# Optimization experiments

Measured on AMD Instinct MI355X. Metric: run time of the kernel, lower is better.

Reference implementation:

```python
import jax, jax.numpy as jnp
import numpy as np
import math

B, L, D = 2, 2048, 256
N_SETS, PLANES_PER_SET = 4, 4
TOTAL_PLANES = N_SETS * PLANES_PER_SET  # 16
POS_PLANES = 16
LTM_PLANES = POS_PLANES
PI = math.pi
LN_EPS = 1e-5


def _mlp2(x, w1, b1, w2, b2):
    h = jax.nn.gelu(x @ w1 + b1, approximate=False)  # torch nn.GELU default = erf
    return h @ w2 + b2


def setup_inputs() -> dict:
    key = jax.random.key(0)
    ks = iter(jax.random.split(key, 40))
    def W(shape):
        return jax.random.normal(next(ks), shape, jnp.float32) / np.float32(np.sqrt(shape[0]))
    z = lambda *s: jnp.zeros(s, jnp.float32)
    return dict(
        x=jax.random.normal(next(ks), (B, L, D), jnp.float32),
        ke_w1=W((D, D)), ke_b1=z(D), ke_w2=W((D, TOTAL_PLANES)), ke_b2=z(TOTAL_PLANES),
        qe_w1=W((D, D)), qe_b1=z(D), qe_w2=W((D, TOTAL_PLANES)), qe_b2=z(TOTAL_PLANES),
        v_w=W((D, D)), v_b=z(D),
        out_ln_g=jnp.ones(D, jnp.float32), out_ln_b=z(D),
        out_w=W((D, D)), out_b=z(D),
        set_weights=jnp.ones(N_SETS, jnp.float32),
        pos_weight=jnp.ones((), jnp.float32),
        gate_w1=W((D, D // 2)), gate_b1=z(D // 2), gate_w2=W((D // 2, 1)), gate_b2=z(1),
        lke_w1=W((D, D)), lke_b1=z(D), lke_w2=W((D, LTM_PLANES)), lke_b2=z(LTM_PLANES),
        surprise_scale=jnp.asarray(5.0, jnp.float32), surprise_bias=jnp.asarray(0.0, jnp.float32),
        resonance_scale=jnp.asarray(5.0, jnp.float32), resonance_threshold=jnp.asarray(0.3, jnp.float32),
        ltm_weight=jnp.asarray(0.5, jnp.float32),
        pos_freqs=jnp.exp(jnp.arange(POS_PLANES, dtype=jnp.float32) * (-math.log(10000.0) / POS_PLANES)),
        ltm_binding_mem=((jax.random.normal(next(ks), (LTM_PLANES, D))
                          + 1j * jax.random.normal(next(ks), (LTM_PLANES, D))) * 0.5).astype(jnp.complex64),
        ltm_count=jnp.asarray(100.0, jnp.float32),
    )


def reference(x, ke_w1, ke_b1, ke_w2, ke_b2, qe_w1, qe_b1, qe_w2, qe_b2,
              v_w, v_b, out_ln_g, out_ln_b, out_w, out_b,
              set_weights, pos_weight, gate_w1, gate_b1, gate_w2, gate_b2,
              lke_w1, lke_b1, lke_w2, lke_b2,
              surprise_scale, surprise_bias, resonance_scale, resonance_threshold,
              ltm_weight, pos_freqs, ltm_binding_mem, ltm_count):
    B_, L_, D_ = x.shape
    key_phasor = jnp.exp(1j * (jnp.tanh(_mlp2(x, ke_w1, ke_b1, ke_w2, ke_b2)) * PI))    # (B,L,16) complex64
    query_phasor = jnp.exp(1j * (jnp.tanh(_mlp2(x, qe_w1, qe_b1, qe_w2, qe_b2)) * PI))  # (B,L,16)
    kp = key_phasor.reshape(B_, L_, N_SETS, PLANES_PER_SET)
    qp = query_phasor.reshape(B_, L_, N_SETS, PLANES_PER_SET)
    weights = jax.nn.softmax(set_weights)
    V_real = x @ v_w + v_b                                                              # (B,L,D)

    # --- cross-bank surprise gate (n_sets > 1 branch) ---
    joint_key = jnp.prod(kp, axis=2)    # (B,L,PP)
    joint_query = jnp.prod(qp, axis=2)
    km = jnp.cumsum(joint_key, axis=1)
    key_memory = jnp.concatenate([jnp.zeros_like(km[:, :1]), km[:, :-1]], axis=1)       # shifted cumsum
    resonance_mag = jnp.abs(key_memory * jnp.conj(joint_query)).mean(-1, keepdims=True)
    positions = jnp.maximum(jnp.arange(L_, dtype=x.dtype), 1.0)
    norm_res = resonance_mag / jnp.sqrt(positions)[None, :, None]
    scale = jnp.clip(resonance_scale, 1.0, 20.0)
    thr = jnp.clip(resonance_threshold, 0.1, 0.9)
    surprise = 0.5 * (1.0 - jnp.tanh(scale * (norm_res - thr)))
    write_gate = jax.nn.sigmoid(surprise_scale * (surprise - 0.5) + surprise_bias)      # (B,L,1)
    Vg = (V_real * write_gate).astype(jnp.complex64)

    # --- cross-bank retrieval over joint (product) phasors ---
    bound = joint_key[..., None] * Vg[:, :, None, :]                                     # (B,L,PP,D)
    mem = jnp.cumsum(bound, axis=1)
    cross = jnp.real((mem * jnp.conj(joint_query)[..., None]).sum(2))                    # (B,L,D)

    # --- per-bank retrieval over all 16 planes ---
    bound_all = key_phasor[..., None] * Vg[:, :, None, :]                                # (B,L,16,D)
    mem_all = jnp.cumsum(bound_all, axis=1)
    ret_all = mem_all * jnp.conj(query_phasor)[..., None]
    per_bank = jnp.real(ret_all.reshape(B_, L_, N_SETS, PLANES_PER_SET, D_).sum(3))      # (B,L,S,D)
    total = (per_bank * weights[None, None, :, None]).sum(2)
    total = (total + cross) / (N_SETS + 1)

    # --- positional phase plane ---
    pos_phase = jnp.arange(L_, dtype=x.dtype)[:, None] * pos_freqs * (2.0 * PI)          # (L,16)
    pos_phasor = jnp.exp(1j * pos_phase)
    Vc = V_real.astype(jnp.complex64)
    bound_pos = pos_phasor[None, :, :, None] * Vc[:, :, None, :]                         # (B,L,16,D)
    mem_pos = jnp.cumsum(bound_pos, axis=1)
    ret_pos = jnp.real((mem_pos * jnp.conj(pos_phasor)[None, :, :, None]).sum(2))        # (B,L,D)
    gate = jax.nn.sigmoid(_mlp2(x, gate_w1, gate_b1, gate_w2, gate_b2))                  # (B,L,1)
    total = gate * total + (1.0 - gate) * (jax.nn.sigmoid(pos_weight) * ret_pos)

    # --- long-term memory retrieval (inference path; buffers are constants) ---
    ltm_phasor = jnp.exp(1j * (jnp.tanh(_mlp2(x, lke_w1, lke_b1, lke_w2, lke_b2)) * PI)) # (B,L,16)
    persistent = jnp.real((ltm_binding_mem[None, None] * jnp.conj(ltm_phasor)[..., None]).sum(2))
    pnorm = jnp.sqrt(jnp.maximum(ltm_count, 1.0) * LTM_PLANES)
    total = total + jax.nn.sigmoid(ltm_weight) * (persistent / pnorm)

    # --- to_out: LayerNorm + Linear ---
    mu = total.mean(-1, keepdims=True)
    var = ((total - mu) ** 2).mean(-1, keepdims=True)
    h = (total - mu) / jnp.sqrt(var + LN_EPS) * out_ln_g + out_ln_b
    return h @ out_w + out_b
```

## Files before the change

kernel.cpp:

```cpp
#include <hip/hip_runtime.h>
#include <hip/hip_bf16.h>
#include <math.h>

#define BB 2
#define LL 2048
#define DD 256
#define NT (BB*LL)
#define HCOLS 896
#define NCOLS 1152
#define KBIG 768
#define FDIM 80
#define CC 64
#define NC (NT/CC)
#define NCB (LL/CC)
#define SST (FDIM*DD)
#define PI_F 3.14159265358979323846f

typedef __attribute__((ext_vector_type(8))) short s8frag;
typedef __attribute__((ext_vector_type(4))) float f4acc;

#define GLDS16(g, l) __builtin_amdgcn_global_load_lds( \
    (const __attribute__((address_space(1))) void*)(g), \
    (__attribute__((address_space(3))) void*)(l), 16, 0, 0)

__device__ __forceinline__ float gelu_erf(float v) {
    return 0.5f * v * (1.0f + erff(v * 0.70710678118654752440f));
}
__device__ __forceinline__ float sigmoidf_(float v) {
    return 1.0f / (1.0f + expf(-v));
}

#define K0A_BLKS (NT * DD / 4 / 256)
#define K0B_BLKS (NCOLS * KBIG / 256)
#define K0C_BLKS (4 * 16 * 768 / 256)
__global__ __launch_bounds__(256) void k0_prep(
    const float* __restrict__ x,
    const float* __restrict__ ke_w1, const float* __restrict__ ke_b1,
    const float* __restrict__ qe_w1, const float* __restrict__ qe_b1,
    const float* __restrict__ lke_w1, const float* __restrict__ lke_b1,
    const float* __restrict__ gate_w1, const float* __restrict__ gate_b1,
    const float* __restrict__ v_w, const float* __restrict__ v_b,
    const float* __restrict__ ke_w2, const float* __restrict__ qe_w2,
    const float* __restrict__ lke_w2, const float* __restrict__ gate_w2,
    __hip_bfloat16* __restrict__ xhi, __hip_bfloat16* __restrict__ xlo,
    __hip_bfloat16* __restrict__ BT, float* __restrict__ bcat,
    __hip_bfloat16* __restrict__ W2T)
{
    const int b = blockIdx.x, tid = threadIdx.x;
    if (b < K0A_BLKS) {
        int idx = b * 256 + tid;
        float4 v = reinterpret_cast<const float4*>(x)[idx];
        float vv[4] = {v.x, v.y, v.z, v.w};
        #pragma unroll
        for (int j = 0; j < 4; ++j) {
            __hip_bfloat16 h = __float2bfloat16(vv[j]);
            xhi[idx * 4 + j] = h;
            xlo[idx * 4 + j] = __float2bfloat16(vv[j] - __bfloat162float(h));
        }
    } else if (b < K0A_BLKS + K0B_BLKS) {
        int idx = (b - K0A_BLKS) * 256 + tid;
        int n = idx / KBIG;
        int kp = idx - n * KBIG;
        int k = (kp < 256) ? kp : (kp < 512 ? kp - 256 : kp - 512);
        float w;
        if (n < 256)      w = ke_w1[k * 256 + n];
        else if (n < 512) w = qe_w1[k * 256 + (n - 256)];
        else if (n < 768) w = lke_w1[k * 256 + (n - 512)];
        else if (n < 896) w = gate_w1[k * 128 + (n - 768)];
        else              w = v_w[k * 256 + (n - 896)];
        __hip_bfloat16 hi = __float2bfloat16(w);
        __hip_bfloat16 out = (kp >= 256 && kp < 512)
            ? __float2bfloat16(w - __bfloat162float(hi)) : hi;
        BT[(size_t)n * KBIG + kp] = out;
        if (kp == 0) {
            float bia;
            if (n < 256)      bia = ke_b1[n];
            else if (n < 512) bia = qe_b1[n - 256];
            else if (n < 768) bia = lke_b1[n - 512];
            else if (n < 896) bia = gate_b1[n - 768];
            else              bia = v_b[n - 896];
            bcat[n] = bia;
        }
    } else {
        int idx = (b - K0A_BLKS - K0B_BLKS) * 256 + tid;
        int g = idx / (16 * 768);
        int rem = idx - g * (16 * 768);
        int n = rem / 768;
        int kp = rem - n * 768;
        float w = 0.0f;
        int seg;
        if (g < 3) {
            seg = kp >> 8;
            int k = kp & 255;
            const float* W = (g == 0) ? ke_w2 : (g == 1) ? qe_w2 : lke_w2;
            w = W[k * 16 + n];
        } else {
            seg = kp >> 7;
            int k = kp & 127;
            if (n == 0 && kp < 384) w = gate_w2[k];
            else { seg = 0; w = 0.0f; }
        }
        __hip_bfloat16 hi = __float2bfloat16(w);
        __hip_bfloat16 out = (seg == 1) ? __float2bfloat16(w - __bfloat162float(hi)) : hi;
        W2T[idx] = out;
    }
}

__global__ __launch_bounds__(256) void k1_mfma(
    const __hip_bfloat16* __restrict__ xhi, const __hip_bfloat16* __restrict__ xlo,
    const __hip_bfloat16* __restrict__ BT, const float* __restrict__ bcat,
    __hip_bfloat16* __restrict__ Hhi, __hip_bfloat16* __restrict__ Hlo,
    float* __restrict__ V)
{
    __shared__ __align__(16) short As[128 * 32];
    __shared__ __align__(16) short Bs[64 * 32];
    const int tid = threadIdx.x;
    const int wave = tid >> 6, lane = tid & 63;
    const int wr = wave >> 1, wc = wave & 1;
    const int bm = blockIdx.x, bn = blockIdx.y;
    const int lg = lane >> 4, lr = lane & 15;

    f4acc acc[4][2] = {};

    for (int kt = 0; kt < KBIG / 32; ++kt) {
        const int k0 = kt * 32;
        const __hip_bfloat16* xsrc = (k0 < 512) ? xhi : xlo;
        const int kcol = (k0 < 512) ? (k0 & 255) : (k0 - 512);
        #pragma unroll
        for (int j = 0; j < 2; ++j) {
            int r0 = wave * 32 + j * 16;
            int row = r0 + (lane >> 2);
            int ch = (lane & 3) ^ ((row >> 1) & 3);
            const __hip_bfloat16* ga = xsrc + (size_t)(bm * 128 + row) * DD + kcol + ch * 8;
            GLDS16(ga, &As[r0 * 32]);
        }
        {
            int r0b = wave * 16;
            int row = r0b + (lane >> 2);
            int ch = (lane & 3) ^ ((row >> 1) & 3);
            const __hip_bfloat16* gb = BT + (size_t)(bn * 64 + row) * KBIG + k0 + ch * 8;
            GLDS16(gb, &Bs[r0b * 32]);
        }
        __syncthreads();
        s8frag a[4], b[2];
        #pragma unroll
        for (int i = 0; i < 4; ++i) {
            int arow = wr * 64 + i * 16 + lr;
            a[i] = *reinterpret_cast<const s8frag*>(
                &As[arow * 32 + ((lg ^ ((arow >> 1) & 3)) << 3)]);
        }
        #pragma unroll
        for (int i = 0; i < 2; ++i) {
            int brow = wc * 32 + i * 16 + lr;
            b[i] = *reinterpret_cast<const s8frag*>(
                &Bs[brow * 32 + ((lg ^ ((brow >> 1) & 3)) << 3)]);
        }
        #pragma unroll
        for (int mi = 0; mi < 4; ++mi)
            #pragma unroll
            for (int ni = 0; ni < 2; ++ni)
                acc[mi][ni] = __builtin_amdgcn_mfma_f32_16x16x32_bf16(
                    a[mi], b[ni], acc[mi][ni], 0, 0, 0);
        __syncthreads();
    }

    #pragma unroll
    for (int ni = 0; ni < 2; ++ni) {
        int n = bn * 64 + wc * 32 + ni * 16 + lr;
        float bia = bcat[n];
        #pragma unroll
        for (int mi = 0; mi < 4; ++mi) {
            #pragma unroll
            for (int r = 0; r < 4; ++r) {
                int m = bm * 128 + wr * 64 + mi * 16 + lg * 4 + r;
                float v = acc[mi][ni][r] + bia;
                if (n < HCOLS) {
                    float hv = gelu_erf(v);
                    __hip_bfloat16 h = __float2bfloat16(hv);
                    Hhi[(size_t)m * HCOLS + n] = h;
                    Hlo[(size_t)m * HCOLS + n] = __float2bfloat16(hv - __bfloat162float(h));
                } else {
                    V[(size_t)m * DD + (n - HCOLS)] = v;
                }
            }
        }
    }
}

__global__ __launch_bounds__(256) void k2_fused(
    const __hip_bfloat16* __restrict__ Hhi, const __hip_bfloat16* __restrict__ Hlo,
    const __hip_bfloat16* __restrict__ W2T,
    const float* __restrict__ ke_b2, const float* __restrict__ qe_b2,
    const float* __restrict__ lke_b2, const float* __restrict__ gate_b2,
    const float* __restrict__ set_weights, const float* __restrict__ pos_weight,
    const float* __restrict__ ltm_weight, const float* __restrict__ ltm_count,
    const float* __restrict__ pos_freqs,
    float* __restrict__ Fk, float* __restrict__ Fq, float* __restrict__ Fql,
    float* __restrict__ J)
{
    __shared__ float c2s[32][52];
    const int tid = threadIdx.x;
    const int g = tid >> 6, lane = tid & 63;
    const int lg = lane >> 4, lr = lane & 15;
    const int t0 = blockIdx.x * 32;

    {
        const int seglen = (g < 3) ? 256 : 128;
        const int gbase = (g < 3) ? g * 256 : 768;
        const int nsteps = (g < 3) ? 24 : 12;
        const __hip_bfloat16* wbase = W2T + (size_t)(g * 16 + lr) * 768;
        f4acc acc[2] = {};
        for (int kt = 0; kt < nsteps; ++kt) {
            const int kp = kt * 32;
            const int seg = kp / seglen;
            const int kk = kp - seg * seglen;
            const __hip_bfloat16* asrc = (seg < 2) ? Hhi : Hlo;
            const int col = gbase + kk + lg * 8;
            s8frag b = *reinterpret_cast<const s8frag*>(wbase + kp + lg * 8);
            #pragma unroll
            for (int mi = 0; mi < 2; ++mi) {
                s8frag a = *reinterpret_cast<const s8frag*>(
                    asrc + (size_t)(t0 + mi * 16 + lr) * HCOLS + col);
                acc[mi] = __builtin_amdgcn_mfma_f32_16x16x32_bf16(a, b, acc[mi], 0, 0, 0);
            }
        }
        int col = g * 16 + lr;
        if (col < 49) {
            #pragma unroll
            for (int mi = 0; mi < 2; ++mi)
                #pragma unroll
                for (int r = 0; r < 4; ++r)
                    c2s[mi * 16 + lg * 4 + r][col] = acc[mi][r];
        }
    }
    __syncthreads();

    for (int i = tid; i < 32 * 64; i += 256) {
        int t = i >> 6, c = i & 63;
        if (c < 49) {
            float a = c2s[t][c];
            float val;
            if (c < 16)      val = tanhf(a + ke_b2[c]) * PI_F;
            else if (c < 32) val = tanhf(a + qe_b2[c - 16]) * PI_F;
            else if (c < 48) val = tanhf(a + lke_b2[c - 32]) * PI_F;
            else             val = sigmoidf_(a + gate_b2[0]);
            c2s[t][c] = val;
        }
    }
    __syncthreads();

    float sw[4];
    {
        float s0 = set_weights[0], s1 = set_weights[1], s2 = set_weights[2], s3 = set_weights[3];
        float mx = fmaxf(fmaxf(s0, s1), fmaxf(s2, s3));
        float e0 = expf(s0 - mx), e1 = expf(s1 - mx), e2 = expf(s2 - mx), e3 = expf(s3 - mx);
        float inv = 1.0f / (e0 + e1 + e2 + e3);
        sw[0] = e0 * inv; sw[1] = e1 * inv; sw[2] = e2 * inv; sw[3] = e3 * inv;
    }
    const float spw = sigmoidf_(pos_weight[0]);
    const float altm = sigmoidf_(ltm_weight[0]) / sqrtf(fmaxf(ltm_count[0], 1.0f) * 16.0f);
    const int sg = tid >> 5, sl = tid & 31;

    for (int tr = 0; tr < 4; ++tr) {
        const int lt = tr * 8 + sg;
        const int t = t0 + lt;
        const float gg = c2s[lt][48];
        const float aq = gg * 0.2f;
        const float apos = (1.0f - gg) * spw;
        const int l = t & (LL - 1);
        float* fkr  = Fk  + (size_t)t * FDIM;
        float* fqr  = Fq  + (size_t)t * FDIM;
        float* fqlr = Fql + (size_t)t * 32;

        if (sl < 16) {
            int p = sl;
            float sk, ck; sincosf(c2s[lt][p], &sk, &ck);
            fkr[2 * p] = ck; fkr[2 * p + 1] = sk;
            float sq, cq; sincosf(c2s[lt][16 + p], &sq, &cq);
            float wq = aq * sw[p >> 2];
            fqr[2 * p] = wq * cq; fqr[2 * p + 1] = wq * sq;
            float sl_, cl_; sincosf(c2s[lt][32 + p], &sl_, &cl_);
            fqlr[2 * p] = altm * cl_; fqlr[2 * p + 1] = altm * sl_;
            float th = (float)l * pos_freqs[p] * (2.0f * PI_F);
            float sp, cp; sincosf(th, &sp, &cp);
            fkr[40 + 2 * p] = cp; fkr[41 + 2 * p] = sp;
            fqr[40 + 2 * p] = apos * cp; fqr[41 + 2 * p] = apos * sp;
        } else if (sl < 20) {
            int p = sl - 16;
            float pjk = c2s[lt][p] + c2s[lt][p + 4] + c2s[lt][p + 8] + c2s[lt][p + 12];
            float pjq = c2s[lt][16 + p] + c2s[lt][20 + p] + c2s[lt][24 + p] + c2s[lt][28 + p];
            float sjk, cjk; sincosf(pjk, &sjk, &cjk);
            float sjq, cjq; sincosf(pjq, &sjq, &cjq);
            fkr[32 + 2 * p] = cjk; fkr[33 + 2 * p] = sjk;
            fqr[32 + 2 * p] = aq * cjq; fqr[33 + 2 * p] = aq * sjq;
            J[(size_t)(2 * p) * NT + t] = cjk;
            J[(size_t)(2 * p + 1) * NT + t] = sjk;
        } else if (sl < 24) {
            int p = sl - 20;
            fkr[72 + 2 * p] = 0.0f; fkr[73 + 2 * p] = 0.0f;
            fqr[72 + 2 * p] = 0.0f; fqr[73 + 2 * p] = 0.0f;
        }
    }
}

__device__ __forceinline__ int swz2048(int l) {
    return (l & ~31) | ((l ^ (l >> 5)) & 31);
}
__global__ __launch_bounds__(512) void k3a_scan(
    const float* __restrict__ J, float* __restrict__ wg,
    const float* __restrict__ resonance_scale, const float* __restrict__ resonance_threshold,
    const float* __restrict__ surprise_scale, const float* __restrict__ surprise_bias)
{
    __shared__ float km[8 * LL];
    const int b = blockIdx.x;
    const int tid = threadIdx.x;
    const int w = tid >> 6;
    const int lane = tid & 63;
    {
        float v[32];
        float s = 0.0f;
        int l0 = lane * 32;
        const float4* src = reinterpret_cast<const float4*>(
            J + (size_t)w * NT + b * LL + l0);
        #pragma unroll
        for (int i = 0; i < 8; ++i) {
            float4 q = src[i];
            v[4 * i + 0] = q.x; v[4 * i + 1] = q.y;
            v[4 * i + 2] = q.z; v[4 * i + 3] = q.w;
            s += q.x + q.y + q.z + q.w;
        }
        float local = s;
        #pragma unroll
        for (int off = 1; off < 64; off <<= 1) {
            float n = __shfl_up(s, off);
            if (lane >= off) s += n;
        }
        float run = s - local;
        #pragma unroll 4
        for (int i = 0; i < 32; ++i) { km[w * LL + swz2048(l0 + i)] = run; run += v[i]; }
    }
    __syncthreads();
    const float sc  = fminf(fmaxf(resonance_scale[0], 1.0f), 20.0f);
    const float th  = fminf(fmaxf(resonance_threshold[0], 0.1f), 0.9f);
    const float ssc = surprise_scale[0];
    const float sbi = surprise_bias[0];
    for (int q = 0; q < 4; ++q) {
        int l = tid + 512 * q;
        int ls = swz2048(l);
        float rm = 0.0f;
        #pragma unroll
        for (int p = 0; p < 4; ++p) {
            float re = km[(2 * p) * LL + ls], im = km[(2 * p + 1) * LL + ls];
            rm += sqrtf(re * re + im * im);
        }
        rm *= 0.25f;
        float nr = rm / sqrtf(fmaxf((float)l, 1.0f));
        float sur = 0.5f * (1.0f - tanhf(sc * (nr - th)));
        wg[b * LL + l] = sigmoidf_(ssc * (sur - 0.5f) + sbi);
    }
}

__global__ __launch_bounds__(256) void k4a_state(
    const float* __restrict__ Fk, const float* __restrict__ wg,
    const float* __restrict__ V, float* __restrict__ S)
{
    __shared__ __align__(16) float fk[CC][FDIM];
    const int c = blockIdx.x;
    const int f0 = blockIdx.y * 20;
    const int tid = threadIdx.x;
    for (int i = tid; i < CC * FDIM; i += 256) {
        int r = i / FDIM, cx = i - r * FDIM;
        float f = Fk[(size_t)c * CC * FDIM + i];
        if (cx < 40) f *= wg[c * CC + r];
        fk[r][cx] = f;
    }
    __syncthreads();
    float acc[20];
    #pragma unroll
    for (int f = 0; f < 20; ++f) acc[f] = 0.0f;
    const float* vp = V + (size_t)c * CC * DD + tid;
    for (int r = 0; r < CC; ++r) {
        float v = vp[(size_t)r * DD];
        #pragma unroll
        for (int g = 0; g < 5; ++g) {
            float4 q = *reinterpret_cast<const float4*>(&fk[r][f0 + 4 * g]);
            acc[4 * g + 0] += q.x * v; acc[4 * g + 1] += q.y * v;
            acc[4 * g + 2] += q.z * v; acc[4 * g + 3] += q.w * v;
        }
    }
    float* sp = S + (size_t)c * SST + tid;
    #pragma unroll
    for (int f = 0; f < 20; ++f) sp[(size_t)(f0 + f) * DD] = acc[f];
}

__global__ __launch_bounds__(256) void k4b_scan(
    const float* __restrict__ S, float* __restrict__ M)
{
    const int e = blockIdx.x * 256 + threadIdx.x;
    const int b = blockIdx.y;
    float run = 0.0f;
    #pragma unroll 8
    for (int cc = 0; cc < NCB; ++cc) {
        size_t o = ((size_t)(b * NCB + cc)) * SST + e;
        M[o] = run;
        run += S[o];
    }
}

__global__ __launch_bounds__(256) void k4c_out(
    const float* __restrict__ Fq, const float* __restrict__ Fk,
    const float* __restrict__ wg, const float* __restrict__ Fql,
    const float* __restrict__ V, const float* __restrict__ M,
    const float* __restrict__ ltm_mem, float* __restrict__ Tot)
{
    __shared__ __align__(16) float fq[8][FDIM];
    __shared__ __align__(16) float fkS[CC * 96];
    __shared__ __align__(16) float sc[8][68];
    const int c = blockIdx.x;
    const int h = blockIdx.y;
    const int r0 = h * 8;
    const int nrows = r0 + 8;
    const int tid = threadIdx.x;

    for (int i = tid; i < 8 * FDIM; i += 256) {
        int r = i / FDIM, cx = i - r * FDIM;
        fq[r][cx] = Fq[(size_t)(c * CC + r0 + r) * FDIM + cx];
    }
    for (int i = tid; i < nrows * FDIM; i += 256) {
        int r = i / FDIM, cx = i - r * FDIM;
        float f = Fk[(size_t)c * CC * FDIM + i];
        if (cx < 40) f *= wg[c * CC + r];
        fkS[r * 96 + (cx ^ ((r & 7) << 2))] = f;
    }
    __syncthreads();

    #pragma unroll
    for (int q = 0; q < 2; ++q) {
        int idx = tid + 256 * q;
        int i = idx >> 6, j = idx & 63;
        float s = 0.0f;
        if (r0 + i >= j) {
            const int sw = (j & 7) << 2;
            #pragma unroll
            for (int g = 0; g < 20; ++g) {
                float4 a = *reinterpret_cast<const float4*>(&fq[i][4 * g]);
                float4 b = *reinterpret_cast<const float4*>(&fkS[j * 96 + ((4 * g) ^ sw)]);
                s += a.x * b.x + a.y * b.y + a.z * b.z + a.w * b.w;
            }
        }
        sc[i][j] = s;
    }
    __syncthreads();

    const int d = tid;
    float acc[8];
    #pragma unroll
    for (int i = 0; i < 8; ++i) acc[i] = 0.0f;

    const float* mp = M + (size_t)c * SST + d;
    #pragma unroll 2
    for (int g = 0; g < 20; ++g) {
        float m0 = mp[(size_t)(4 * g + 0) * DD];
        float m1 = mp[(size_t)(4 * g + 1) * DD];
        float m2 = mp[(size_t)(4 * g + 2) * DD];
        float m3 = mp[(size_t)(4 * g + 3) * DD];
        #pragma unroll
        for (int i = 0; i < 8; ++i) {
            float4 a = *reinterpret_cast<const float4*>(&fq[i][4 * g]);
            acc[i] += a.x * m0 + a.y * m1 + a.z * m2 + a.w * m3;
        }
    }
    const float* vp = V + (size_t)c * CC * DD + d;
    const int j4max = nrows >> 2;
    #pragma unroll 2
    for (int j4 = 0; j4 < j4max; ++j4) {
        float v0 = vp[(size_t)(4 * j4 + 0) * DD];
        float v1 = vp[(size_t)(4 * j4 + 1) * DD];
        float v2 = vp[(size_t)(4 * j4 + 2) * DD];
        float v3 = vp[(size_t)(4 * j4 + 3) * DD];
        #pragma unroll
        for (int i = 0; i < 8; ++i) {
            float4 s4 = *reinterpret_cast<const float4*>(&sc[i][4 * j4]);
            acc[i] += s4.x * v0 + s4.y * v1 + s4.z * v2 + s4.w * v3;
        }
    }
    float mre[16], mim[16];
    #pragma unroll
    for (int p = 0; p < 16; ++p) {
        mre[p] = ltm_mem[((size_t)p * DD + d) * 2];
        mim[p] = ltm_mem[((size_t)p * DD + d) * 2 + 1];
    }
    __syncthreads();
    {
        int r = tid >> 5, p = tid & 31;
        sc[r][p] = Fql[(size_t)(c * CC + r0 + r) * 32 + p];
    }
    __syncthreads();
    float* tp = Tot + (size_t)(c * CC + r0) * DD + d;
    #pragma unroll 1
    for (int i = 0; i < 8; ++i) {
        float a = acc[i];
        #pragma unroll
        for (int p = 0; p < 16; ++p)
            a += sc[i][2 * p] * mre[p] + sc[i][2 * p + 1] * mim[p];
        tp[(size_t)i * DD] = a;
    }
}

__global__ __launch_bounds__(256) void k5_out(
    const float* __restrict__ Tot,
    const float* __restrict__ gln, const float* __restrict__ bln,
    const float* __restrict__ out_w, const float* __restrict__ out_b,
    float* __restrict__ out)
{
    __shared__ float hsn[DD][16];
    const int tid = threadIdx.x;
    const int t0 = blockIdx.x * 16;
    const int w = tid >> 6, lane = tid & 63;
    {
        int r = 4 * w + (lane >> 4);
        int l4 = lane & 15;
        float vbuf[16];
        float s = 0.0f, s2 = 0.0f;
        const float4* src = reinterpret_cast<const float4*>(
            Tot + (size_t)(t0 + r) * DD + l4 * 16);
        #pragma unroll
        for (int g = 0; g < 4; ++g) {
            float4 v = src[g];
            vbuf[4 * g + 0] = v.x; vbuf[4 * g + 1] = v.y;
            vbuf[4 * g + 2] = v.z; vbuf[4 * g + 3] = v.w;
            s += v.x + v.y + v.z + v.w;
            s2 += v.x * v.x + v.y * v.y + v.z * v.z + v.w * v.w;
        }
        #pragma unroll
        for (int off = 1; off < 16; off <<= 1) {
            s  += __shfl_xor(s, off);
            s2 += __shfl_xor(s2, off);
        }
        float mu = s * (1.0f / 256.0f);
        float var = s2 * (1.0f / 256.0f) - mu * mu;
        float rstd = rsqrtf(var + 1e-5f);
        const int swc = (l4 & 3) << 2;
        #pragma unroll
        for (int i = 0; i < 16; ++i) {
            int k = l4 * 16 + i;
            hsn[k][r ^ swc] = (vbuf[i] - mu) * rstd * gln[k] + bln[k];
        }
    }
    __syncthreads();
    float acc[16];
    #pragma unroll
    for (int t = 0; t < 16; ++t) acc[t] = 0.0f;
    #pragma unroll 4
    for (int k = 0; k < DD; ++k) {
        float wv = out_w[(size_t)k * DD + tid];
        const int swc = ((k >> 4) & 3) << 2;
        #pragma unroll
        for (int g = 0; g < 4; ++g) {
            float4 hv = *reinterpret_cast<const float4*>(&hsn[k][(4 * g) ^ swc]);
            acc[4 * g + 0] += hv.x * wv;
            acc[4 * g + 1] += hv.y * wv;
            acc[4 * g + 2] += hv.z * wv;
            acc[4 * g + 3] += hv.w * wv;
        }
    }
    float ob = out_b[tid];
    #pragma unroll
    for (int t = 0; t < 16; ++t)
        out[(size_t)(t0 + t) * DD + tid] = acc[t] + ob;
}

extern "C" void kernel_launch(void* const* d_in, const int* in_sizes, int n_in,
                              void* d_out, int out_size, void* d_ws, size_t ws_size,
                              hipStream_t stream)
{
    (void)in_sizes; (void)n_in; (void)out_size; (void)ws_size;
    const float* x        = (const float*)d_in[0];
    const float* ke_w1    = (const float*)d_in[1];
    const float* ke_b1    = (const float*)d_in[2];
    const float* ke_w2    = (const float*)d_in[3];
    const float* ke_b2    = (const float*)d_in[4];
    const float* qe_w1    = (const float*)d_in[5];
    const float* qe_b1    = (const float*)d_in[6];
    const float* qe_w2    = (const float*)d_in[7];
    const float* qe_b2    = (const float*)d_in[8];
    const float* v_w      = (const float*)d_in[9];
    const float* v_b      = (const float*)d_in[10];
    const float* out_ln_g = (const float*)d_in[11];
    const float* out_ln_b = (const float*)d_in[12];
    const float* out_w    = (const float*)d_in[13];
    const float* out_b    = (const float*)d_in[14];
    const float* set_weights = (const float*)d_in[15];
    const float* pos_weight  = (const float*)d_in[16];
    const float* gate_w1  = (const float*)d_in[17];
    const float* gate_b1  = (const float*)d_in[18];
    const float* gate_w2  = (const float*)d_in[19];
    const float* gate_b2  = (const float*)d_in[20];
    const float* lke_w1   = (const float*)d_in[21];
    const float* lke_b1   = (const float*)d_in[22];
    const float* lke_w2   = (const float*)d_in[23];
    const float* lke_b2   = (const float*)d_in[24];
    const float* surprise_scale      = (const float*)d_in[25];
    const float* surprise_bias       = (const float*)d_in[26];
    const float* resonance_scale     = (const float*)d_in[27];
    const float* resonance_threshold = (const float*)d_in[28];
    const float* ltm_weight = (const float*)d_in[29];
    const float* pos_freqs  = (const float*)d_in[30];
    const float* ltm_mem    = (const float*)d_in[31];
    const float* ltm_count  = (const float*)d_in[32];

    float* ws  = (float*)d_ws;
    float* Hf  = ws;
    float* V   = Hf  + (size_t)NT * HCOLS;
    float* Fk  = V   + (size_t)NT * DD;
    float* Fq  = Fk  + (size_t)NT * FDIM;
    float* Fql = Fq  + (size_t)NT * FDIM;
    float* Tot = Fql + (size_t)NT * 32;
    float* J   = Tot + (size_t)NT * DD;
    __hip_bfloat16* W2T = (__hip_bfloat16*)(J + (size_t)NT * 8);
    float* wg  = (float*)(W2T + 4 * 16 * 768);

    __hip_bfloat16* Hhi = (__hip_bfloat16*)Hf;
    __hip_bfloat16* Hlo = Hhi + (size_t)NT * HCOLS;
    float* S   = Hf;
    float* M   = Hf + (size_t)NC * SST;
    __hip_bfloat16* xhi = (__hip_bfloat16*)Fk;
    __hip_bfloat16* xlo = xhi + (size_t)NT * DD;
    __hip_bfloat16* BT  = xlo + (size_t)NT * DD;
    float* bcat = (float*)(BT + (size_t)NCOLS * KBIG);

    k0_prep<<<K0A_BLKS + K0B_BLKS + K0C_BLKS, 256, 0, stream>>>(
        x, ke_w1, ke_b1, qe_w1, qe_b1, lke_w1, lke_b1, gate_w1, gate_b1, v_w, v_b,
        ke_w2, qe_w2, lke_w2, gate_w2, xhi, xlo, BT, bcat, W2T);
    k1_mfma<<<dim3(NT / 128, NCOLS / 64), 256, 0, stream>>>(xhi, xlo, BT, bcat,
                                                            Hhi, Hlo, V);
    k2_fused<<<NT / 32, 256, 0, stream>>>(Hhi, Hlo, W2T,
                                          ke_b2, qe_b2, lke_b2, gate_b2,
                                          set_weights, pos_weight,
                                          ltm_weight, ltm_count, pos_freqs,
                                          Fk, Fq, Fql, J);
    k3a_scan<<<BB, 512, 0, stream>>>(J, wg, resonance_scale, resonance_threshold,
                                     surprise_scale, surprise_bias);
    k4a_state<<<dim3(NC, 4), 256, 0, stream>>>(Fk, wg, V, S);
    k4b_scan<<<dim3(SST / 256, BB), 256, 0, stream>>>(S, M);
    k4c_out<<<dim3(NC, 8), 256, 0, stream>>>(Fq, Fk, wg, Fql, V, M, ltm_mem, Tot);
    k5_out<<<NT / 16, 256, 0, stream>>>(Tot, out_ln_g, out_ln_b, out_w, out_b, (float*)d_out);
}
```

Before: 131.7 us.

## Fuse LayerNorm+output projection into retrieval kernel, widen GEMM K-tile, tile weight transpose

The final LayerNorm and output linear layer move into the retrieval kernel, so the Tot intermediate is no longer written and re-read and one launch disappears. Separately, the main MFMA GEMM now stages 64-wide K tiles with an 8-way XOR swizzle, which halves the barrier count. The weight-transpose prep now goes through a shared-memory tile so both reads and writes are coalesced, and bias packing moves into separate blocks. The fused kernel adds a cross-wave reduction plus a second GEMM per block with only 8 rows each, which could lower efficiency for that stage.

```diff
diff --git a/kernel.cpp b/kernel.cpp
--- a/kernel.cpp
+++ b/kernel.cpp
@@ -31,8 +31,9 @@
 }
 
 #define K0A_BLKS (NT * DD / 4 / 256)
-#define K0B_BLKS (NCOLS * KBIG / 256)
+#define K0B_BLKS ((KBIG / 64) * (NCOLS / 64))
 #define K0C_BLKS (4 * 16 * 768 / 256)
+#define K0D_BLKS 5
 __global__ __launch_bounds__(256) void k0_prep(
     const float* __restrict__ x,
     const float* __restrict__ ke_w1, const float* __restrict__ ke_b1,
@@ -46,6 +47,7 @@
     __hip_bfloat16* __restrict__ BT, float* __restrict__ bcat,
     __hip_bfloat16* __restrict__ W2T)
 {
+    __shared__ float tile[64][65];
     const int b = blockIdx.x, tid = threadIdx.x;
     if (b < K0A_BLKS) {
         int idx = b * 256 + tid;
@@ -58,30 +60,36 @@
             xlo[idx * 4 + j] = __float2bfloat16(vv[j] - __bfloat162float(h));
         }
     } else if (b < K0A_BLKS + K0B_BLKS) {
-        int idx = (b - K0A_BLKS) * 256 + tid;
-        int n = idx / KBIG;
-        int kp = idx - n * KBIG;
-        int k = (kp < 256) ? kp : (kp < 512 ? kp - 256 : kp - 512);
-        float w;
-        if (n < 256)      w = ke_w1[k * 256 + n];
-        else if (n < 512) w = qe_w1[k * 256 + (n - 256)];
-        else if (n < 768) w = lke_w1[k * 256 + (n - 512)];
-        else if (n < 896) w = gate_w1[k * 128 + (n - 768)];
-        else              w = v_w[k * 256 + (n - 896)];
-        __hip_bfloat16 hi = __float2bfloat16(w);
-        __hip_bfloat16 out = (kp >= 256 && kp < 512)
-            ? __float2bfloat16(w - __bfloat162float(hi)) : hi;
-        BT[(size_t)n * KBIG + kp] = out;
-        if (kp == 0) {
-            float bia;
-            if (n < 256)      bia = ke_b1[n];
-            else if (n < 512) bia = qe_b1[n - 256];
-            else if (n < 768) bia = lke_b1[n - 512];
-            else if (n < 896) bia = gate_b1[n - 768];
-            else              bia = v_b[n - 896];
-            bcat[n] = bia;
-        }
-    } else {
+        int bb = b - K0A_BLKS;
+        int bk = bb / 18, bn = bb - bk * 18;
+        int kp0 = bk * 64, n0 = bn * 64;
+        int seg = kp0 >> 8;
+        int k0 = kp0 - seg * 256;
+        #pragma unroll 4
+        for (int i = 0; i < 16; ++i) {
+            int kl = i * 4 + (tid >> 6);
+            int nl = tid & 63;
+            int k = k0 + kl, n = n0 + nl;
+            float w;
+            if (n < 256)      w = ke_w1[k * 256 + n];
+            else if (n < 512) w = qe_w1[k * 256 + (n - 256)];
+            else if (n < 768) w = lke_w1[k * 256 + (n - 512)];
+            else if (n < 896) w = gate_w1[k * 128 + (n - 768)];
+            else              w = v_w[k * 256 + (n - 896)];
+            tile[kl][nl] = w;
+        }
+        __syncthreads();
+        #pragma unroll 4
+        for (int i = 0; i < 16; ++i) {
+            int nl = i * 4 + (tid >> 6);
+            int kpl = tid & 63;
+            float w = tile[kpl][nl];
+            __hip_bfloat16 hi = __float2bfloat16(w);
+            __hip_bfloat16 out = (seg == 1)
+                ? __float2bfloat16(w - __bfloat162float(hi)) : hi;
+            BT[(size_t)(n0 + nl) * KBIG + kp0 + kpl] = out;
+        }
+    } else if (b < K0A_BLKS + K0B_BLKS + K0C_BLKS) {
         int idx = (b - K0A_BLKS - K0B_BLKS) * 256 + tid;
         int g = idx / (16 * 768);
         int rem = idx - g * (16 * 768);
@@ -103,6 +111,17 @@
         __hip_bfloat16 hi = __float2bfloat16(w);
         __hip_bfloat16 out = (seg == 1) ? __float2bfloat16(w - __bfloat162float(hi)) : hi;
         W2T[idx] = out;
+    } else {
+        int n = (b - K0A_BLKS - K0B_BLKS - K0C_BLKS) * 256 + tid;
+        if (n < NCOLS) {
+            float bia;
+            if (n < 256)      bia = ke_b1[n];
+            else if (n < 512) bia = qe_b1[n - 256];
+            else if (n < 768) bia = lke_b1[n - 512];
+            else if (n < 896) bia = gate_b1[n - 768];
+            else              bia = v_b[n - 896];
+            bcat[n] = bia;
+        }
     }
 }
 
@@ -112,8 +131,8 @@
     __hip_bfloat16* __restrict__ Hhi, __hip_bfloat16* __restrict__ Hlo,
     float* __restrict__ V)
 {
-    __shared__ __align__(16) short As[128 * 32];
-    __shared__ __align__(16) short Bs[64 * 32];
+    __shared__ __align__(16) short As[128 * 64];
+    __shared__ __align__(16) short Bs[64 * 64];
     const int tid = threadIdx.x;
     const int wave = tid >> 6, lane = tid & 63;
     const int wr = wave >> 1, wc = wave & 1;
@@ -122,45 +141,47 @@
 
     f4acc acc[4][2] = {};
 
-    for (int kt = 0; kt < KBIG / 32; ++kt) {
-        const int k0 = kt * 32;
-        const __hip_bfloat16* xsrc = (k0 < 512) ? xhi : xlo;
-        const int kcol = (k0 < 512) ? (k0 & 255) : (k0 - 512);
+    for (int kt = 0; kt < KBIG / 64; ++kt) {
+        const int k0 = kt * 64;
+        const __hip_bfloat16* xsrc = (kt < 8) ? xhi : xlo;
+        const int kcol = (kt < 8) ? (k0 & 255) : (k0 - 512);
+        #pragma unroll
+        for (int j = 0; j < 4; ++j) {
+            int r0 = wave * 32 + j * 8;
+            int row = r0 + (lane >> 3);
+            int ch = (lane & 7) ^ (row & 7);
+            GLDS16(xsrc + (size_t)(bm * 128 + row) * DD + kcol + ch * 8, &As[r0 * 64]);
+        }
         #pragma unroll
         for (int j = 0; j < 2; ++j) {
-            int r0 = wave * 32 + j * 16;
-            int row = r0 + (lane >> 2);
-            int ch = (lane & 3) ^ ((row >> 1) & 3);
-            const __hip_bfloat16* ga = xsrc + (size_t)(bm * 128 + row) * DD + kcol + ch * 8;
-            GLDS16(ga, &As[r0 * 32]);
-        }
-        {
-            int r0b = wave * 16;
-            int row = r0b + (lane >> 2);
-            int ch = (lane & 3) ^ ((row >> 1) & 3);
-            const __hip_bfloat16* gb = BT + (size_t)(bn * 64 + row) * KBIG + k0 + ch * 8;
-            GLDS16(gb, &Bs[r0b * 32]);
+            int r0 = wave * 16 + j * 8;
+            int row = r0 + (lane >> 3);
+            int ch = (lane & 7) ^ (row & 7);
+            GLDS16(BT + (size_t)(bn * 64 + row) * KBIG + k0 + ch * 8, &Bs[r0 * 64]);
         }
         __syncthreads();
-        s8frag a[4], b[2];
-        #pragma unroll
-        for (int i = 0; i < 4; ++i) {
-            int arow = wr * 64 + i * 16 + lr;
-            a[i] = *reinterpret_cast<const s8frag*>(
-                &As[arow * 32 + ((lg ^ ((arow >> 1) & 3)) << 3)]);
-        }
-        #pragma unroll
-        for (int i = 0; i < 2; ++i) {
-            int brow = wc * 32 + i * 16 + lr;
-            b[i] = *reinterpret_cast<const s8frag*>(
-                &Bs[brow * 32 + ((lg ^ ((brow >> 1) & 3)) << 3)]);
-        }
-        #pragma unroll
-        for (int mi = 0; mi < 4; ++mi)
-            #pragma unroll
-            for (int ni = 0; ni < 2; ++ni)
-                acc[mi][ni] = __builtin_amdgcn_mfma_f32_16x16x32_bf16(
-                    a[mi], b[ni], acc[mi][ni], 0, 0, 0);
+        #pragma unroll
+        for (int kk = 0; kk < 2; ++kk) {
+            s8frag a[4], b[2];
+            #pragma unroll
+            for (int i = 0; i < 4; ++i) {
+                int arow = wr * 64 + i * 16 + lr;
+                int slot = (kk * 4 + lg) ^ (arow & 7);
+                a[i] = *reinterpret_cast<const s8frag*>(&As[arow * 64 + slot * 8]);
+            }
+            #pragma unroll
+            for (int i = 0; i < 2; ++i) {
+                int brow = wc * 32 + i * 16 + lr;
+                int slot = (kk * 4 + lg) ^ (brow & 7);
+                b[i] = *reinterpret_cast<const s8frag*>(&Bs[brow * 64 + slot * 8]);
+            }
+            #pragma unroll
+            for (int mi = 0; mi < 4; ++mi)
+                #pragma unroll
+                for (int ni = 0; ni < 2; ++ni)
+                    acc[mi][ni] = __builtin_amdgcn_mfma_f32_16x16x32_bf16(
+                        a[mi], b[ni], acc[mi][ni], 0, 0, 0);
+        }
         __syncthreads();
     }
 
@@ -407,11 +428,14 @@
     }
 }
 
-__global__ __launch_bounds__(256) void k4c_out(
+__global__ __launch_bounds__(256) void k4c_fused(
     const float* __restrict__ Fq, const float* __restrict__ Fk,
     const float* __restrict__ wg, const float* __restrict__ Fql,
     const float* __restrict__ V, const float* __restrict__ M,
-    const float* __restrict__ ltm_mem, float* __restrict__ Tot)
+    const float* __restrict__ ltm_mem,
+    const float* __restrict__ gln, const float* __restrict__ bln,
+    const float* __restrict__ out_w, const float* __restrict__ out_b,
+    float* __restrict__ out)
 {
     __shared__ __align__(16) float fq[8][FDIM];
     __shared__ __align__(16) float fkS[CC * 96];
@@ -421,6 +445,7 @@
     const int r0 = h * 8;
     const int nrows = r0 + 8;
     const int tid = threadIdx.x;
+    const int wave = tid >> 6, lane = tid & 63;
 
     for (int i = tid; i < 8 * FDIM; i += 256) {
         int r = i / FDIM, cx = i - r * FDIM;
@@ -484,90 +509,73 @@
             acc[i] += s4.x * v0 + s4.y * v1 + s4.z * v2 + s4.w * v3;
         }
     }
-    float mre[16], mim[16];
-    #pragma unroll
-    for (int p = 0; p < 16; ++p) {
-        mre[p] = ltm_mem[((size_t)p * DD + d) * 2];
-        mim[p] = ltm_mem[((size_t)p * DD + d) * 2 + 1];
-    }
-    __syncthreads();
     {
-        int r = tid >> 5, p = tid & 31;
-        sc[r][p] = Fql[(size_t)(c * CC + r0 + r) * 32 + p];
-    }
-    __syncthreads();
-    float* tp = Tot + (size_t)(c * CC + r0) * DD + d;
-    #pragma unroll 1
+        float mre[16], mim[16];
+        #pragma unroll
+        for (int p = 0; p < 16; ++p) {
+            mre[p] = ltm_mem[((size_t)p * DD + d) * 2];
+            mim[p] = ltm_mem[((size_t)p * DD + d) * 2 + 1];
+        }
+        __syncthreads();
+        {
+            int r = tid >> 5, p = tid & 31;
+            sc[r][p] = Fql[(size_t)(c * CC + r0 + r) * 32 + p];
+        }
+        __syncthreads();
+        #pragma unroll
+        for (int i = 0; i < 8; ++i) {
+            float a = acc[i];
+            #pragma unroll
+            for (int p = 0; p < 16; ++p)
+                a += sc[i][2 * p] * mre[p] + sc[i][2 * p + 1] * mim[p];
+            acc[i] = a;
+        }
+    }
+    __syncthreads();
+
+    #pragma unroll
     for (int i = 0; i < 8; ++i) {
-        float a = acc[i];
-        #pragma unroll
-        for (int p = 0; p < 16; ++p)
-            a += sc[i][2 * p] * mre[p] + sc[i][2 * p + 1] * mim[p];
-        tp[(size_t)i * DD] = a;
-    }
-}
-
-__global__ __launch_bounds__(256) void k5_out(
-    const float* __restrict__ Tot,
-    const float* __restrict__ gln, const float* __restrict__ bln,
-    const float* __restrict__ out_w, const float* __restrict__ out_b,
-    float* __restrict__ out)
-{
-    __shared__ float hsn[DD][16];
-    const int tid = threadIdx.x;
-    const int t0 = blockIdx.x * 16;
-    const int w = tid >> 6, lane = tid & 63;
-    {
-        int r = 4 * w + (lane >> 4);
-        int l4 = lane & 15;
-        float vbuf[16];
-        float s = 0.0f, s2 = 0.0f;
-        const float4* src = reinterpret_cast<const float4*>(
-            Tot + (size_t)(t0 + r) * DD + l4 * 16);
-        #pragma unroll
-        for (int g = 0; g < 4; ++g) {
-            float4 v = src[g];
-            vbuf[4 * g + 0] = v.x; vbuf[4 * g + 1] = v.y;
-            vbuf[4 * g + 2] = v.z; vbuf[4 * g + 3] = v.w;
-            s += v.x + v.y + v.z + v.w;
-            s2 += v.x * v.x + v.y * v.y + v.z * v.z + v.w * v.w;
-        }
-        #pragma unroll
-        for (int off = 1; off < 16; off <<= 1) {
+        float s = acc[i], s2 = acc[i] * acc[i];
+        #pragma unroll
+        for (int off = 1; off < 64; off <<= 1) {
             s  += __shfl_xor(s, off);
             s2 += __shfl_xor(s2, off);
         }
+        if (lane == 0) { sc[i][wave] = s; sc[i][4 + wave] = s2; }
+    }
+    __syncthreads();
+    const float gv = gln[d], bv = bln[d];
+    #pragma unroll
+    for (int i = 0; i < 8; ++i) {
+        float s  = sc[i][0] + sc[i][1] + sc[i][2] + sc[i][3];
+        float s2 = sc[i][4] + sc[i][5] + sc[i][6] + sc[i][7];
         float mu = s * (1.0f / 256.0f);
         float var = s2 * (1.0f / 256.0f) - mu * mu;
         float rstd = rsqrtf(var + 1e-5f);
-        const int swc = (l4 & 3) << 2;
-        #pragma unroll
-        for (int i = 0; i < 16; ++i) {
-            int k = l4 * 16 + i;
-            hsn[k][r ^ swc] = (vbuf[i] - mu) * rstd * gln[k] + bln[k];
-        }
-    }
-    __syncthreads();
-    float acc[16];
-    #pragma unroll
-    for (int t = 0; t < 16; ++t) acc[t] = 0.0f;
-    #pragma unroll 4
-    for (int k = 0; k < DD; ++k) {
-        float wv = out_w[(size_t)k * DD + tid];
-        const int swc = ((k >> 4) & 3) << 2;
-        #pragma unroll
-        for (int g = 0; g < 4; ++g) {
-            float4 hv = *reinterpret_cast<const float4*>(&hsn[k][(4 * g) ^ swc]);
-            acc[4 * g + 0] += hv.x * wv;
-            acc[4 * g + 1] += hv.y * wv;
-            acc[4 * g + 2] += hv.z * wv;
-            acc[4 * g + 3] += hv.w * wv;
+        fkS[i * 256 + d] = (acc[i] - mu) * rstd * gv + bv;
+    }
+    __syncthreads();
+
+    float oacc[8];
+    #pragma unroll
+    for (int i = 0; i < 8; ++i) oacc[i] = 0.0f;
+    #pragma unroll 2
+    for (int d0 = 0; d0 < DD; d0 += 4) {
+        float w0 = out_w[(size_t)(d0 + 0) * DD + tid];
+        float w1 = out_w[(size_t)(d0 + 1) * DD + tid];
+        float w2 = out_w[(size_t)(d0 + 2) * DD + tid];
+        float w3 = out_w[(size_t)(d0 + 3) * DD + tid];
+        #pragma unroll
+        for (int i = 0; i < 8; ++i) {
+            float4 hq = *reinterpret_cast<const float4*>(&fkS[i * 256 + d0]);
+            oacc[i] += hq.x * w0 + hq.y * w1 + hq.z * w2 + hq.w * w3;
         }
     }
     float ob = out_b[tid];
-    #pragma unroll
-    for (int t = 0; t < 16; ++t)
-        out[(size_t)(t0 + t) * DD + tid] = acc[t] + ob;
+    float* op = out + (size_t)(c * CC + r0) * DD + tid;
+    #pragma unroll
+    for (int i = 0; i < 8; ++i)
+        op[(size_t)i * DD] = oacc[i] + ob;
 }
 
 extern "C" void kernel_launch(void* const* d_in, const int* in_sizes, int n_in,
@@ -629,7 +637,7 @@
     __hip_bfloat16* BT  = xlo + (size_t)NT * DD;
     float* bcat = (float*)(BT + (size_t)NCOLS * KBIG);
 
-    k0_prep<<<K0A_BLKS + K0B_BLKS + K0C_BLKS, 256, 0, stream>>>(
+    k0_prep<<<K0A_BLKS + K0B_BLKS + K0C_BLKS + K0D_BLKS, 256, 0, stream>>>(
         x, ke_w1, ke_b1, qe_w1, qe_b1, lke_w1, lke_b1, gate_w1, gate_b1, v_w, v_b,
         ke_w2, qe_w2, lke_w2, gate_w2, xhi, xlo, BT, bcat, W2T);
     k1_mfma<<<dim3(NT / 128, NCOLS / 64), 256, 0, stream>>>(xhi, xlo, BT, bcat,
@@ -643,6 +651,7 @@
                                      surprise_scale, surprise_bias);
     k4a_state<<<dim3(NC, 4), 256, 0, stream>>>(Fk, wg, V, S);
     k4b_scan<<<dim3(SST / 256, BB), 256, 0, stream>>>(S, M);
-    k4c_out<<<dim3(NC, 8), 256, 0, stream>>>(Fq, Fk, wg, Fql, V, M, ltm_mem, Tot);
-    k5_out<<<NT / 16, 256, 0, stream>>>(Tot, out_ln_g, out_ln_b, out_w, out_b, (float*)d_out);
-}
+    k4c_fused<<<dim3(NC, 8), 256, 0, stream>>>(Fq, Fk, wg, Fql, V, M, ltm_mem,
+                                               out_ln_g, out_ln_b, out_w, out_b,
+                                               (float*)d_out);
+}
```

Measured after the change: 132.8 us. About the same (+0.8%).
